# Optimization experiments

Hardware: AMD Instinct MI355X
Metric: run time of the kernel (lower is better)

The kernel has to match this reference:

```python
import jax, jax.numpy as jnp
import numpy as np

V = 16000   # src/trg vocab
E = 512     # embedding dim (encoder_dim = decoder_dim)
H = 512     # hidden_size
L = 2       # n_layers
S = 128     # src len
T = 128     # trg len
B = 64      # batch


def _lstm_stack(x, Wih, Whh, bih, bhh, h0, c0):
    """Multi-layer LSTM, PyTorch gate order (i, f, g, o).
    x: [T, B, E]; Wih/Whh: [L, 4H, *]; bih/bhh: [L, 4H]; h0/c0: [L, B, H].
    Returns (outputs [T,B,H], hN [L,B,H], cN [L,B,H]). Dropout is eval-mode (identity)."""
    inp = x
    hs, cs = [], []
    for l in range(Wih.shape[0]):
        W1, W2 = Wih[l], Whh[l]
        b = bih[l] + bhh[l]
        def step(carry, xt, W1=W1, W2=W2, b=b):
            h, c = carry
            g = xt @ W1.T + h @ W2.T + b          # [B, 4H]
            i, f, gg, o = jnp.split(g, 4, axis=-1)
            c = jax.nn.sigmoid(f) * c + jax.nn.sigmoid(i) * jnp.tanh(gg)
            h = jax.nn.sigmoid(o) * jnp.tanh(c)
            return (h, c), h
        (h, c), ys = jax.lax.scan(step, (h0[l], c0[l]), inp)
        inp = ys
        hs.append(h)
        cs.append(c)
    return inp, jnp.stack(hs), jnp.stack(cs)


def setup_inputs() -> dict:
    key = jax.random.key(0)
    ks = jax.random.split(key, 16)
    u = lambda k, shape: jax.random.uniform(k, shape, jnp.float32, -0.08, 0.08)
    inp = {
        "src": jax.random.randint(ks[0], (S, B), 0, V),
        "trg": jax.random.randint(ks[1], (T, B), 0, V),
        "teacher_forcing_ratio": 1,
        "enc_emb": u(ks[2], (V, E)),
        "dec_emb": u(ks[3], (V, E)),
        "enc_Wih": jnp.stack([u(ks[4], (4 * H, E)), u(ks[5], (4 * H, H))]),
        "enc_Whh": u(ks[6], (L, 4 * H, H)),
        "enc_bih": u(ks[7], (L, 4 * H)),
        "enc_bhh": u(ks[8], (L, 4 * H)),
        "dec_Wih": jnp.stack([u(ks[9], (4 * H, E)), u(ks[10], (4 * H, H))]),
        "dec_Whh": u(ks[11], (L, 4 * H, H)),
        "dec_bih": u(ks[12], (L, 4 * H)),
        "dec_bhh": u(ks[13], (L, 4 * H)),
        "out_W": u(ks[14], (V, H)),
        "out_b": u(ks[15], (V,)),
    }
    return inp


def reference(src, trg, teacher_forcing_ratio, enc_emb, dec_emb,
              enc_Wih, enc_Whh, enc_bih, enc_bhh,
              dec_Wih, dec_Whh, dec_bih, dec_bhh, out_W, out_b):
    # Encoder: embed + 2-layer LSTM over src; keep final (h, c).
    zeros = jnp.zeros((L, B, H), enc_emb.dtype)
    _, h, c = _lstm_stack(enc_emb[src], enc_Wih, enc_Whh, enc_bih, enc_bhh, zeros, zeros)
    # Decoder: teacher_forcing_ratio=1 => input at step t is trg[t-1];
    # the per-step python loop collapses to one LSTM scan over trg[:-1].
    dec_in = dec_emb[trg[:-1]]                    # [T-1, B, E]
    ys, _, _ = _lstm_stack(dec_in, dec_Wih, dec_Whh, dec_bih, dec_bhh, h, c)
    logits = jnp.einsum('tbh,vh->tbv', ys, out_W) + out_b   # [T-1, B, V]
    # original: outputs[1:].view(-1, V)
    return logits.reshape(-1, V)
```

## Files before the change

kernel.cpp:

```cpp
#include <hip/hip_runtime.h>


typedef __attribute__((ext_vector_type(8))) short v8s;
typedef __attribute__((ext_vector_type(4))) short v4s;
typedef __attribute__((ext_vector_type(8))) _Float16 v8h;
typedef __attribute__((ext_vector_type(4))) float v4f;
typedef __attribute__((ext_vector_type(4))) unsigned int v4u;

#define AS1 __attribute__((address_space(1)))
#define AS3 __attribute__((address_space(3)))

__device__ __forceinline__ short f2h(float x) {
  _Float16 h = (_Float16)x;
  return __builtin_bit_cast(short, h);
}
__device__ __forceinline__ void gload16(const void* g, void* l) {
  __builtin_amdgcn_global_load_lds((const AS1 void*)g, (AS3 void*)l, 16, 0, 0);
}
__device__ __forceinline__ float sigf(float x) { return 1.f / (1.f + __expf(-x)); }
__device__ __forceinline__ float tanhfast(float x) { return 2.f / (1.f + __expf(-2.f * x)) - 1.f; }

__device__ __forceinline__ void ld16_sc1(v4u& d, const void* p) {
  asm volatile("global_load_dwordx4 %0, %1, off sc1" : "=v"(d) : "v"(p) : "memory");
}
__device__ __forceinline__ void ld16(v4u& d, const void* p) {
  asm volatile("global_load_dwordx4 %0, %1, off" : "=v"(d) : "v"(p));
}

__device__ __forceinline__ void poll32(const unsigned* flags, int base, unsigned tgt) {
  int lane = threadIdx.x & 63;
  const unsigned* fp = flags + base + (lane & 31);
  while (true) {
    unsigned v;
    asm volatile("global_load_dword %0, %1, off sc1\n\ts_waitcnt vmcnt(0)"
                 : "=v"(v) : "v"(fp) : "memory");
    if (__all((int)((lane >= 32) || (v >= tgt)))) break;
    __builtin_amdgcn_s_sleep(1);
  }
}

__global__ void conv_w(const float* __restrict__ in, short* __restrict__ out,
                       int rows, int ldo, int coloff, int reorder) {
  int i = blockIdx.x * 256 + threadIdx.x;
  if (i >= rows * 128) return;
  int r = i >> 7, k4 = (i & 127) * 4;
  int rr = reorder ? (((r >> 4) & 31) * 64 + (r >> 9) * 16 + (r & 15)) : r;
  float4 v = *(const float4*)(in + (size_t)r * 512 + k4);
  v4s s; s[0] = f2h(v.x); s[1] = f2h(v.y); s[2] = f2h(v.z); s[3] = f2h(v.w);
  *(v4s*)(out + (size_t)rr * ldo + coloff + k4) = s;
}

__global__ void conv_b(const float* __restrict__ a, const float* __restrict__ b,
                       float* __restrict__ o) {
  int r = blockIdx.x * 256 + threadIdx.x;
  if (r < 2048) o[((r >> 4) & 31) * 64 + (r >> 9) * 16 + (r & 15)] = a[r] + b[r];
}

__global__ void embed_k(const int* __restrict__ ids, const float* __restrict__ emb,
                        short* __restrict__ out, int nvalid) {
  int row = blockIdx.x;
  int e = threadIdx.x * 2;
  float2 v = make_float2(0.f, 0.f);
  if (row < nvalid) {
    int id = ids[row];
    v = *(const float2*)(emb + (size_t)id * 512 + e);
  }
  unsigned pack = ((unsigned)(unsigned short)f2h(v.y) << 16) | (unsigned short)f2h(v.x);
  *(unsigned*)(out + (size_t)row * 512 + e) = pack;
}

__global__ void zero_k(short* p, int n) {
  int i = blockIdx.x * 256 + threadIdx.x;
  if (i < n) p[i] = 0;
}

#define GF_BIAS 2
#define GF_GUARDM 4

__global__ __launch_bounds__(256, 2) void gemm_bt(
    const short* __restrict__ Am, const short* __restrict__ Bm,
    const float* __restrict__ bias, float* __restrict__ Cm,
    int M, int N, int K, int ldc, int flags) {
  __shared__ short lA[128 * 64];
  __shared__ short lB[128 * 64];
  const int tid = threadIdx.x, lane = tid & 63, wave = tid >> 6;
  const int wm = wave >> 1, wn = wave & 1;
  const int tm = blockIdx.y, tn = blockIdx.x;
  v4f acc[4][4] = {};
  const short* Abase = Am + (size_t)tm * 128 * K;
  const short* Bbase = Bm + (size_t)tn * 128 * K;

  for (int kt = 0; kt < K; kt += 64) {
    __syncthreads();
#pragma unroll
    for (int i2 = 0; i2 < 4; ++i2) {
      int c = (wave * 4 + i2) * 64 + lane;
      int row = c >> 3, ch = c & 7;
      int sch = ch ^ (row & 7);
      gload16(Abase + (size_t)row * K + kt + sch * 8, (char*)lA + (wave * 4 + i2) * 1024);
      gload16(Bbase + (size_t)row * K + kt + sch * 8, (char*)lB + (wave * 4 + i2) * 1024);
    }
    asm volatile("s_waitcnt vmcnt(0)" ::: "memory");
    __syncthreads();
#pragma unroll
    for (int kc = 0; kc < 2; ++kc) {
      v8h af[4], bh[4];
#pragma unroll
      for (int mt = 0; mt < 4; ++mt) {
        int row = wm * 64 + mt * 16 + (lane & 15);
        af[mt] = *(const v8h*)((const char*)lA + row * 128 +
                               ((kc * 64 + (lane >> 4) * 16) ^ ((row & 7) << 4)));
      }
#pragma unroll
      for (int nt = 0; nt < 4; ++nt) {
        int row = wn * 64 + nt * 16 + (lane & 15);
        bh[nt] = *(const v8h*)((const char*)lB + row * 128 +
                               ((kc * 64 + (lane >> 4) * 16) ^ ((row & 7) << 4)));
      }
#pragma unroll
      for (int mt = 0; mt < 4; ++mt)
#pragma unroll
        for (int nt = 0; nt < 4; ++nt)
          acc[mt][nt] = __builtin_amdgcn_mfma_f32_16x16x32_f16(af[mt], bh[nt], acc[mt][nt], 0, 0, 0);
    }
  }

  const int rbase = tm * 128 + wm * 64 + (lane >> 4) * 4;
  const int cbase = tn * 128 + wn * 64 + (lane & 15);
#pragma unroll
  for (int mt = 0; mt < 4; ++mt) {
#pragma unroll
    for (int nt = 0; nt < 4; ++nt) {
      int gc = cbase + nt * 16;
      float bv = (flags & GF_BIAS) ? bias[gc] : 0.f;
#pragma unroll
      for (int rg = 0; rg < 4; ++rg) {
        int gr = rbase + mt * 16 + rg;
        if ((flags & GF_GUARDM) && gr >= M) continue;
        Cm[(size_t)gr * ldc + gc] = acc[mt][nt][rg] + bv;
      }
    }
  }
}

struct PipeArgs {
  const short* W0e;
  const short* W0d;
  const short* W1e;
  const short* W1d;
  const short* X;
  const float* b0e;
  const float* b0d;
  const float* b1e;
  const float* b1d;
  short* h0;
  short* h1;
  unsigned* flags;
  int Tenc, Ttot;
};

#define SLOT 32768

__global__ __launch_bounds__(256, 1) void lstm_pipe(PipeArgs A) {
  __shared__ __align__(16) short Wlds[64 * 1024];
  __shared__ __align__(16) short hsm[64 * 16];
  const int tid = threadIdx.x, lane = tid & 63, wave = tid >> 6;
  const int w = blockIdx.x, layer = w >> 5, wl = w & 31;

  auto stage = [&](const short* Wsrc) {
    for (int i = tid * 8; i < 64 * 1024; i += 256 * 8) {
      int row = i >> 10, k = i & 1023;
      v8s v = *(const v8s*)(Wsrc + (size_t)row * 1024 + k);
      *(v8s*)((char*)Wlds + row * 2048 + ((k * 2) ^ ((row & 7) << 4))) = v;
    }
  };
  stage((layer ? A.W1e : A.W0e) + (size_t)(wl * 64) * 1024);

  const int uu = lane & 15;
  float beV[4], bdV[4];
#pragma unroll
  for (int g = 0; g < 4; ++g) {
    beV[g] = (layer ? A.b1e : A.b0e)[wl * 64 + g * 16 + uu];
    bdV[g] = (layer ? A.b1d : A.b0d)[wl * 64 + g * 16 + uu];
  }
  float creg[4] = {0.f, 0.f, 0.f, 0.f};

  const int arow = wave * 16 + uu;
  const int koff = (lane >> 4) * 8;
  const size_t aoff = (size_t)arow * 512 + koff;
  __syncthreads();

  for (int t = 0; t < A.Ttot; ++t) {
    if (t == A.Tenc) {
      stage((layer ? A.W1d : A.W0d) + (size_t)(wl * 64) * 1024);
      __syncthreads();
    }

    v4f acc[4] = {};

    if (layer) {
      if (wave == 0) poll32(A.flags, 0, (unsigned)(t + 1));
      __syncthreads();
    }
    {
      const short* p1 = (layer ? (A.h0 + (size_t)(t + 1) * SLOT)
                               : (A.X + (size_t)t * SLOT)) + aoff;
      v4u fa[16];
      if (layer) {
#pragma unroll
        for (int kc = 0; kc < 16; ++kc) ld16_sc1(fa[kc], p1 + kc * 32);
      } else {
#pragma unroll
        for (int kc = 0; kc < 16; ++kc) ld16(fa[kc], p1 + kc * 32);
      }
      asm volatile("s_waitcnt vmcnt(0)" ::: "memory");
      __builtin_amdgcn_sched_barrier(0);
#pragma unroll
      for (int kc = 0; kc < 16; ++kc) {
        v8h af = __builtin_bit_cast(v8h, fa[kc]);
        int kg = kc * 32 + koff;
#pragma unroll
        for (int nt = 0; nt < 4; ++nt) {
          int wrow = nt * 16 + uu;
          v8h bh = *(const v8h*)((const char*)Wlds + wrow * 2048 +
                                 ((kg * 2) ^ ((wrow & 7) << 4)));
          acc[nt] = __builtin_amdgcn_mfma_f32_16x16x32_f16(af, bh, acc[nt], 0, 0, 0);
        }
      }
    }

    if (t > 0) {
      if (wave == 0) poll32(A.flags, layer ? 32 : 0, (unsigned)t);
      __syncthreads();
    }
    {
      const short* p2 = ((layer ? A.h1 : A.h0) + (size_t)t * SLOT) + aoff;
      v4u fb[16];
#pragma unroll
      for (int kc = 0; kc < 16; ++kc) ld16_sc1(fb[kc], p2 + kc * 32);
      asm volatile("s_waitcnt vmcnt(0)" ::: "memory");
      __builtin_amdgcn_sched_barrier(0);
#pragma unroll
      for (int kc = 0; kc < 16; ++kc) {
        v8h af = __builtin_bit_cast(v8h, fb[kc]);
        int kg = (kc + 16) * 32 + koff;
#pragma unroll
        for (int nt = 0; nt < 4; ++nt) {
          int wrow = nt * 16 + uu;
          v8h bh = *(const v8h*)((const char*)Wlds + wrow * 2048 +
                                 ((kg * 2) ^ ((wrow & 7) << 4)));
          acc[nt] = __builtin_amdgcn_mfma_f32_16x16x32_f16(af, bh, acc[nt], 0, 0, 0);
        }
      }
    }

    {
      const bool enc = t < A.Tenc;
      const float b0v = enc ? beV[0] : bdV[0];
      const float b1v = enc ? beV[1] : bdV[1];
      const float b2v = enc ? beV[2] : bdV[2];
      const float b3v = enc ? beV[3] : bdV[3];
#pragma unroll
      for (int rg = 0; rg < 4; ++rg) {
        float g0 = acc[0][rg] + b0v;
        float g1 = acc[1][rg] + b1v;
        float g2 = acc[2][rg] + b2v;
        float g3 = acc[3][rg] + b3v;
        float c = sigf(g1) * creg[rg] + sigf(g0) * tanhfast(g2);
        creg[rg] = c;
        float h = sigf(g3) * tanhfast(c);
        int bb = wave * 16 + ((lane >> 4) << 2) + rg;
        hsm[bb * 16 + uu] = f2h(h);
      }
    }
    __syncthreads();

    if (tid < 128) {
      int b = tid >> 1, half = tid & 1;
      v4u d = *(const v4u*)(&hsm[b * 16 + half * 8]);
      short* dst = (layer ? A.h1 : A.h0) + (size_t)(t + 1) * SLOT
                   + b * 512 + wl * 16 + half * 8;
      asm volatile("global_store_dwordx4 %0, %1, off sc1" :: "v"(dst), "v"(d) : "memory");
    }
    asm volatile("s_waitcnt vmcnt(0)" ::: "memory");
    __syncthreads();
    if (tid == 0) {
      unsigned val = (unsigned)(t + 1);
      const unsigned* fp = A.flags + w;
      asm volatile("global_store_dword %0, %1, off sc1" :: "v"(fp), "v"(val) : "memory");
    }
  }
}

extern "C" void kernel_launch(void* const* d_in, const int* in_sizes, int n_in,
                              void* d_out, int out_size, void* d_ws, size_t ws_size,
                              hipStream_t stream) {
  (void)in_sizes; (void)n_in; (void)out_size; (void)ws_size;
  const int* src = (const int*)d_in[0];
  const int* trg = (const int*)d_in[1];
  const float* enc_emb = (const float*)d_in[3];
  const float* dec_emb = (const float*)d_in[4];
  const float* enc_Wih = (const float*)d_in[5];
  const float* enc_Whh = (const float*)d_in[6];
  const float* enc_bih = (const float*)d_in[7];
  const float* enc_bhh = (const float*)d_in[8];
  const float* dec_Wih = (const float*)d_in[9];
  const float* dec_Whh = (const float*)d_in[10];
  const float* dec_bih = (const float*)d_in[11];
  const float* dec_bhh = (const float*)d_in[12];
  const float* out_W = (const float*)d_in[13];
  const float* out_b = (const float*)d_in[14];

  char* p = (char*)d_ws;
  auto alloc = [&](size_t sz) { char* r = p; p += (sz + 255) & ~(size_t)255; return r; };
  short* H0 = (short*)alloc((size_t)256 * SLOT * 2);
  short* H1 = (short*)alloc((size_t)257 * SLOT * 2);
  short* W0e = (short*)alloc((size_t)2048 * 1024 * 2);
  short* W0d = (short*)alloc((size_t)2048 * 1024 * 2);
  short* W1e = (short*)alloc((size_t)2048 * 1024 * 2);
  short* W1d = (short*)alloc((size_t)2048 * 1024 * 2);
  short* XO = (short*)alloc((size_t)255 * SLOT * 2);
  float* bE0 = (float*)alloc(2048 * 4);
  float* bE1 = (float*)alloc(2048 * 4);
  float* bD0 = (float*)alloc(2048 * 4);
  float* bD1 = (float*)alloc(2048 * 4);
  unsigned* flags = (unsigned*)alloc(256);

  zero_k<<<128, 256, 0, stream>>>(H0, 32768);
  zero_k<<<128, 256, 0, stream>>>(H1, 32768);
  zero_k<<<128, 256, 0, stream>>>(H1 + (size_t)256 * SLOT, 32768);
  zero_k<<<1, 256, 0, stream>>>((short*)flags, 128);

  conv_w<<<1024, 256, 0, stream>>>(enc_Wih, W0e, 2048, 1024, 0, 1);
  conv_w<<<1024, 256, 0, stream>>>(enc_Whh, W0e, 2048, 1024, 512, 1);
  conv_w<<<1024, 256, 0, stream>>>(dec_Wih, W0d, 2048, 1024, 0, 1);
  conv_w<<<1024, 256, 0, stream>>>(dec_Whh, W0d, 2048, 1024, 512, 1);
  conv_w<<<1024, 256, 0, stream>>>(enc_Wih + (size_t)2048 * 512, W1e, 2048, 1024, 0, 1);
  conv_w<<<1024, 256, 0, stream>>>(enc_Whh + (size_t)2048 * 512, W1e, 2048, 1024, 512, 1);
  conv_w<<<1024, 256, 0, stream>>>(dec_Wih + (size_t)2048 * 512, W1d, 2048, 1024, 0, 1);
  conv_w<<<1024, 256, 0, stream>>>(dec_Whh + (size_t)2048 * 512, W1d, 2048, 1024, 512, 1);
  conv_b<<<8, 256, 0, stream>>>(enc_bih, enc_bhh, bE0);
  conv_b<<<8, 256, 0, stream>>>(enc_bih + 2048, enc_bhh + 2048, bE1);
  conv_b<<<8, 256, 0, stream>>>(dec_bih, dec_bhh, bD0);
  conv_b<<<8, 256, 0, stream>>>(dec_bih + 2048, dec_bhh + 2048, bD1);

  embed_k<<<8192, 256, 0, stream>>>(src, enc_emb, XO, 8192);
  embed_k<<<8128, 256, 0, stream>>>(trg, dec_emb, XO + (size_t)8192 * 512, 8128);

  PipeArgs pa = {W0e, W0d, W1e, W1d, XO, bE0, bD0, bE1, bD1,
                 H0, H1, flags, 128, 255};
  lstm_pipe<<<64, 256, 0, stream>>>(pa);

  short* outWb = XO;
  conv_w<<<8000, 256, 0, stream>>>(out_W, outWb, 16000, 512, 0, 0);

  gemm_bt<<<dim3(125, 64), 256, 0, stream>>>(H1 + (size_t)129 * SLOT, outWb, out_b,
                                             (float*)d_out, 8128, 16000, 512, 16000,
                                             GF_BIAS | GF_GUARDM);
}
```

Measured before the change: 2.311 ms.

## Double GEMM K-tile to 128 and stage epilogue through LDS for vectorized stores

The GEMM K-tile grows from 64 to 128. This halves the number of load/sync iterations per tile, and the XOR swizzle is widened to 16 chunks to match. The epilogue now writes accumulators into shared memory and reads them back as row-contiguous float4s with bias added. That gives coalesced 16-byte global stores instead of scattered 4-byte ones. LDS use rises to 64KB per block, which may limit the two-blocks-per-CU occupancy target, and the float tile staging has no padding, so bank conflicts are possible.

```diff
diff --git a/kernel.cpp b/kernel.cpp
--- a/kernel.cpp
+++ b/kernel.cpp
@@ -81,8 +81,9 @@
     const short* __restrict__ Am, const short* __restrict__ Bm,
     const float* __restrict__ bias, float* __restrict__ Cm,
     int M, int N, int K, int ldc, int flags) {
-  __shared__ short lA[128 * 64];
-  __shared__ short lB[128 * 64];
+  __shared__ __align__(16) char smem[65536];
+  short* lA = (short*)smem;
+  short* lB = (short*)(smem + 32768);
   const int tid = threadIdx.x, lane = tid & 63, wave = tid >> 6;
   const int wm = wave >> 1, wn = wave & 1;
   const int tm = blockIdx.y, tn = blockIdx.x;
@@ -90,32 +91,32 @@
   const short* Abase = Am + (size_t)tm * 128 * K;
   const short* Bbase = Bm + (size_t)tn * 128 * K;
 
-  for (int kt = 0; kt < K; kt += 64) {
+  for (int kt = 0; kt < K; kt += 128) {
     __syncthreads();
 #pragma unroll
-    for (int i2 = 0; i2 < 4; ++i2) {
-      int c = (wave * 4 + i2) * 64 + lane;
-      int row = c >> 3, ch = c & 7;
-      int sch = ch ^ (row & 7);
-      gload16(Abase + (size_t)row * K + kt + sch * 8, (char*)lA + (wave * 4 + i2) * 1024);
-      gload16(Bbase + (size_t)row * K + kt + sch * 8, (char*)lB + (wave * 4 + i2) * 1024);
+    for (int i2 = 0; i2 < 8; ++i2) {
+      int c = (wave * 8 + i2) * 64 + lane;
+      int row = c >> 4, ch = c & 15;
+      int sch = ch ^ (row & 15);
+      gload16(Abase + (size_t)row * K + kt + sch * 8, (char*)lA + c * 16);
+      gload16(Bbase + (size_t)row * K + kt + sch * 8, (char*)lB + c * 16);
     }
     asm volatile("s_waitcnt vmcnt(0)" ::: "memory");
     __syncthreads();
 #pragma unroll
-    for (int kc = 0; kc < 2; ++kc) {
+    for (int kc = 0; kc < 4; ++kc) {
       v8h af[4], bh[4];
 #pragma unroll
       for (int mt = 0; mt < 4; ++mt) {
         int row = wm * 64 + mt * 16 + (lane & 15);
-        af[mt] = *(const v8h*)((const char*)lA + row * 128 +
-                               ((kc * 64 + (lane >> 4) * 16) ^ ((row & 7) << 4)));
+        af[mt] = *(const v8h*)((const char*)lA + row * 256 +
+                               ((kc * 64 + (lane >> 4) * 16) ^ ((row & 15) << 4)));
       }
 #pragma unroll
       for (int nt = 0; nt < 4; ++nt) {
         int row = wn * 64 + nt * 16 + (lane & 15);
-        bh[nt] = *(const v8h*)((const char*)lB + row * 128 +
-                               ((kc * 64 + (lane >> 4) * 16) ^ ((row & 7) << 4)));
+        bh[nt] = *(const v8h*)((const char*)lB + row * 256 +
+                               ((kc * 64 + (lane >> 4) * 16) ^ ((row & 15) << 4)));
       }
 #pragma unroll
       for (int mt = 0; mt < 4; ++mt)
@@ -125,21 +126,31 @@
     }
   }
 
-  const int rbase = tm * 128 + wm * 64 + (lane >> 4) * 4;
-  const int cbase = tn * 128 + wn * 64 + (lane & 15);
-#pragma unroll
-  for (int mt = 0; mt < 4; ++mt) {
-#pragma unroll
-    for (int nt = 0; nt < 4; ++nt) {
-      int gc = cbase + nt * 16;
-      float bv = (flags & GF_BIAS) ? bias[gc] : 0.f;
+  __syncthreads();
+  float* ft = (float*)smem;
+#pragma unroll
+  for (int mt = 0; mt < 4; ++mt)
+#pragma unroll
+    for (int nt = 0; nt < 4; ++nt)
 #pragma unroll
       for (int rg = 0; rg < 4; ++rg) {
-        int gr = rbase + mt * 16 + rg;
-        if ((flags & GF_GUARDM) && gr >= M) continue;
-        Cm[(size_t)gr * ldc + gc] = acc[mt][nt][rg] + bv;
-      }
-    }
+        int r = wm * 64 + mt * 16 + (lane >> 4) * 4 + rg;
+        int c = wn * 64 + nt * 16 + (lane & 15);
+        ft[r * 128 + c] = acc[mt][nt][rg];
+      }
+  __syncthreads();
+  const int c4 = (tid & 31) * 4;
+  const int gcol = tn * 128 + c4;
+  float4 bv = make_float4(0.f, 0.f, 0.f, 0.f);
+  if (flags & GF_BIAS) bv = *(const float4*)(bias + gcol);
+#pragma unroll
+  for (int it = 0; it < 16; ++it) {
+    int r = it * 8 + (tid >> 5);
+    int gr = tm * 128 + r;
+    if ((flags & GF_GUARDM) && gr >= M) continue;
+    float4 v = *(const float4*)(ft + r * 128 + c4);
+    v.x += bv.x; v.y += bv.y; v.z += bv.z; v.w += bv.w;
+    *(float4*)(Cm + (size_t)gr * ldc + gcol) = v;
   }
 }
 
```

After: 2.289 ms. No clear change (-1.0%).
